# Performance work log

Hardware: AMD Instinct MI355X
Metric: run time of the kernel (lower is better)

Reference implementation:

```python
import jax, jax.numpy as jnp
import numpy as np

BN_EPS = 1e-5


def setup_inputs() -> dict:
    key = jax.random.key(0)
    ks = jax.random.split(key, 8)
    B, C, H, W = 2, 512, 64, 64
    Ck, Cv = 256, 256
    x = jax.random.normal(ks[0], (B, C, H, W), jnp.float32)
    # f_key/f_query shared 1x1 conv (kaiming, relu)
    wk = jax.random.normal(ks[1], (Ck, C), jnp.float32) * (2.0 / C) ** 0.5
    bk = jnp.zeros((Ck,), jnp.float32)
    bn_gamma = jax.random.uniform(ks[2], (Ck,), jnp.float32, 0.5, 1.5)
    bn_beta = jax.random.normal(ks[3], (Ck,), jnp.float32) * 0.1
    bn_mean = jax.random.normal(ks[4], (Ck,), jnp.float32) * 0.1
    bn_var = jax.random.uniform(ks[5], (Ck,), jnp.float32, 0.5, 1.5)
    # f_value: 3x3 conv then 1x1 conv
    wv1 = jax.random.normal(ks[6], (Cv, C, 3, 3), jnp.float32) * (2.0 / (C * 9)) ** 0.5
    bv1 = jnp.zeros((Cv,), jnp.float32)
    wv2 = jax.random.normal(ks[7], (Cv, Cv), jnp.float32) * (2.0 / Cv) ** 0.5
    bv2 = jnp.zeros((Cv,), jnp.float32)
    return dict(x=x, wk=wk, bk=bk, bn_gamma=bn_gamma, bn_beta=bn_beta,
                bn_mean=bn_mean, bn_var=bn_var, wv1=wv1, bv1=bv1, wv2=wv2, bv2=bv2)


def reference(x, wk, bk, bn_gamma, bn_beta, bn_mean, bn_var, wv1, bv1, wv2, bv2):
    B, C, H, W = x.shape
    Ck, Cv = wk.shape[0], wv1.shape[0]
    N = H * W
    # f_key == f_query: 1x1 conv + BN (inference form) + ReLU
    feat = jnp.einsum('oc,bchw->bohw', wk, x) + bk[:, None, None]
    scale_bn = (bn_gamma / jnp.sqrt(bn_var + BN_EPS))
    feat = (feat - bn_mean[:, None, None]) * scale_bn[:, None, None] + bn_beta[:, None, None]
    feat = jax.nn.relu(feat).reshape(B, Ck, N)  # [B, Ck, N]
    # sim_map = softmax(Ck^-0.5 * Q^T K); Q and K are the same tensor
    sim_map = jax.nn.softmax(jnp.einsum('bcn,bcm->bnm', feat, feat) * (Ck ** -0.5), axis=-1)
    # f_value: conv3x3 + relu + conv1x1 + relu
    v = jax.lax.conv_general_dilated(x, wv1, (1, 1), 'SAME',
                                     dimension_numbers=('NCHW', 'OIHW', 'NCHW'))
    v = jax.nn.relu(v + bv1[:, None, None])
    v = jax.nn.relu(jnp.einsum('oc,bchw->bohw', wv2, v) + bv2[:, None, None])
    v = v.reshape(B, Cv, N)  # [B, Cv, N]
    context = jnp.einsum('bnm,bcm->bcn', sim_map, v).reshape(B, Cv, H, W)
    return context, sim_map
```

## Files before the change

kernel.cpp:

```cpp
#include <hip/hip_runtime.h>
#include <hip/hip_bf16.h>
#include <stdint.h>

typedef unsigned short u16_t;
typedef __attribute__((ext_vector_type(8))) short short8;
typedef __attribute__((ext_vector_type(4))) float f32x4;
typedef __attribute__((ext_vector_type(4))) unsigned short us4;

__device__ __forceinline__ float bf2f(u16_t u) {
  union { unsigned int i; float f; } c; c.i = ((unsigned int)u) << 16; return c.f;
}
__device__ __forceinline__ u16_t f2bf(float f) {
  union { float f; unsigned int i; } c; c.f = f;
  unsigned int x = c.i;
  unsigned int r = x + 0x7fffu + ((x >> 16) & 1u);
  return (u16_t)(r >> 16);
}

__device__ __forceinline__ void gload_lds16(const u16_t* g, u16_t* l) {
  __builtin_amdgcn_global_load_lds(
      (const __attribute__((address_space(1))) void*)g,
      (__attribute__((address_space(3))) void*)(unsigned int)(uintptr_t)l,
      16, 0, 0);
}

struct Seg {
  const u16_t* Ah;
  const u16_t* Al;
  const u16_t* Bh;
  const u16_t* Bl;
  int boff;
};

struct GemmArgs {
  Seg segs[9];
  int nseg;
  int segs_per_split;
  int K;
  int ldA, ldB;
  long long sA, sB;
  float alpha;
  float* outf;
  long long sOut;
  long long sSplit;
  int ldT;
};

template<int BM, int BN, int MODE, bool PADB, bool SYMM>
__global__ __launch_bounds__(256, 4) void gemm_tn(GemmArgs args) {
  constexpr int FM = BM / 32, FN = BN / 32;
  __shared__ __align__(16) u16_t lAh[4][BM][8];
  __shared__ __align__(16) u16_t lAl[(MODE == 0) ? 4 : 1][BM][8];
  __shared__ __align__(16) u16_t lBh[4][BN][8];
  __shared__ __align__(16) u16_t lBl[(MODE <= 1) ? 4 : 1][BN][8];
  const int tid = threadIdx.x;
  const int wave = tid >> 6, lane = tid & 63;
  const int lhi = lane >> 4, llo = lane & 15;
  const int wr = wave >> 1, wc = wave & 1;
  int nt, mt, b, split;
  if (SYMM) {
    b = blockIdx.z; split = 0;
    int t = blockIdx.x, r = 0;
    while (t >= 32 - r) { t -= 32 - r; ++r; }
    mt = r; nt = r + t;
  } else {
    nt = blockIdx.x; mt = blockIdx.y;
    b = blockIdx.z & 1; split = blockIdx.z >> 1;
  }
  const int row0 = mt * BM, col0 = nt * BN;

  f32x4 acc[FM][FN];
  const f32x4 zero4 = {0.f, 0.f, 0.f, 0.f};
#pragma unroll
  for (int i = 0; i < FM; ++i)
#pragma unroll
    for (int j = 0; j < FN; ++j) acc[i][j] = zero4;

  constexpr int RA = BM / 64;
  constexpr int RB = BN / 64;
  u16_t* aflat_h = &lAh[0][0][0];
  u16_t* aflat_l = &lAl[0][0][0];
  u16_t* bflat_h = &lBh[0][0][0];
  u16_t* bflat_l = &lBl[0][0][0];

  const int s0 = split * args.segs_per_split;
  int s1 = s0 + args.segs_per_split;
  if (s1 > args.nseg) s1 = args.nseg;

  for (int s = s0; s < s1; ++s) {
    const u16_t* Abh = args.segs[s].Ah + (size_t)b * args.sA;
    const u16_t* Abl = args.segs[s].Al + (size_t)b * args.sA;
    const u16_t* Bbh = args.segs[s].Bh + (size_t)b * args.sB;
    const u16_t* Bbl = args.segs[s].Bl + (size_t)b * args.sB;
    const int boff = args.segs[s].boff;
    for (int k0 = 0; k0 < args.K; k0 += 32) {
      __syncthreads();
#pragma unroll
      for (int r = 0; r < RA; ++r) {
        int idx = (r * 4 + wave) * 64 + lane;
        int chunk = idx / BM, m = idx % BM;
        size_t goff = (size_t)(row0 + m) * args.ldA + (k0 + chunk * 8);
        gload_lds16(Abh + goff, aflat_h + (size_t)((r * 4 + wave) * 64) * 8);
        if (MODE == 0)
          gload_lds16(Abl + goff, aflat_l + (size_t)((r * 4 + wave) * 64) * 8);
      }
#pragma unroll
      for (int r = 0; r < RB; ++r) {
        int idx = (r * 4 + wave) * 64 + lane;
        int chunk = idx / BN, n = idx % BN;
        long long rowi;
        if (PADB) {
          int gn = col0 + n;
          rowi = (long long)((gn >> 6) + 1) * 66 + (gn & 63) + 1 + boff;
        } else {
          rowi = col0 + n;
        }
        size_t goff = (size_t)rowi * args.ldB + (k0 + chunk * 8);
        gload_lds16(Bbh + goff, bflat_h + (size_t)((r * 4 + wave) * 64) * 8);
        if (MODE <= 1)
          gload_lds16(Bbl + goff, bflat_l + (size_t)((r * 4 + wave) * 64) * 8);
      }
      __syncthreads();
      short8 afh[FM], afl[FM], bfh[FN], bfl[FN];
#pragma unroll
      for (int i = 0; i < FM; ++i) {
        afh[i] = *(const short8*)&lAh[lhi][wr * (BM / 2) + i * 16 + llo][0];
        if (MODE == 0)
          afl[i] = *(const short8*)&lAl[lhi][wr * (BM / 2) + i * 16 + llo][0];
      }
#pragma unroll
      for (int j = 0; j < FN; ++j) {
        bfh[j] = *(const short8*)&lBh[lhi][wc * (BN / 2) + j * 16 + llo][0];
        if (MODE <= 1)
          bfl[j] = *(const short8*)&lBl[lhi][wc * (BN / 2) + j * 16 + llo][0];
      }
#pragma unroll
      for (int i = 0; i < FM; ++i)
#pragma unroll
        for (int j = 0; j < FN; ++j) {
          f32x4 t = acc[i][j];
          if (MODE <= 1)
            t = __builtin_amdgcn_mfma_f32_16x16x32_bf16(afh[i], bfl[j], t, 0, 0, 0);
          if (MODE == 0)
            t = __builtin_amdgcn_mfma_f32_16x16x32_bf16(afl[i], bfh[j], t, 0, 0, 0);
          t = __builtin_amdgcn_mfma_f32_16x16x32_bf16(afh[i], bfh[j], t, 0, 0, 0);
          acc[i][j] = t;
        }
    }
  }

  float* outp = args.outf + (size_t)split * args.sSplit + (size_t)b * args.sOut;
#pragma unroll
  for (int i = 0; i < FM; ++i) {
    int mb = row0 + wr * (BM / 2) + i * 16 + lhi * 4;
#pragma unroll
    for (int j = 0; j < FN; ++j) {
      int n = col0 + wc * (BN / 2) + j * 16 + llo;
      f32x4 vv = acc[i][j] * args.alpha;
      *(f32x4*)(outp + (size_t)n * args.ldT + mb) = vv;
    }
  }
  if (SYMM) {
    if (nt != mt) {
#pragma unroll
      for (int i = 0; i < FM; ++i) {
        int mb = row0 + wr * (BM / 2) + i * 16 + lhi * 4;
#pragma unroll
        for (int j = 0; j < FN; ++j) {
          int n = col0 + wc * (BN / 2) + j * 16 + llo;
#pragma unroll
          for (int r2 = 0; r2 < 4; ++r2)
            outp[(size_t)(mb + r2) * args.ldT + n] = acc[i][j][r2] * args.alpha;
        }
      }
    }
  }
}

__global__ __launch_bounds__(256) void zeropad(u16_t* __restrict__ xh, u16_t* __restrict__ xl) {
  int rowi = blockIdx.x % 260;
  int b = blockIdx.x / 260;
  int rp;
  if (rowi < 66) rp = rowi;
  else if (rowi < 132) rp = 4290 + (rowi - 66);
  else { int g = (rowi - 132) >> 1; rp = (g + 1) * 66 + ((rowi - 132) & 1) * 65; }
  size_t base = ((size_t)b * 4356 + rp) * 512;
  int t = threadIdx.x;
  const us4 z = {0, 0, 0, 0};
  if (t < 128) *(us4*)(xh + base + (size_t)t * 4) = z;
  else *(us4*)(xl + base + (size_t)(t - 128) * 4) = z;
}

template<int LDT, bool PER_COL>
__global__ __launch_bounds__(256) void reduce_split(
    const float* __restrict__ part, long long sSplit, int ns,
    const float* __restrict__ scale, const float* __restrict__ bias,
    u16_t* __restrict__ oh, u16_t* __restrict__ ol, long long total) {
  long long i = ((long long)blockIdx.x * 256 + threadIdx.x) * 4;
  if (i >= total) return;
  f32x4 s = *(const f32x4*)(part + i);
  for (int p = 1; p < ns; ++p) s += *(const f32x4*)(part + (size_t)p * sSplit + i);
  f32x4 v;
  if (PER_COL) {
    int c = (int)(i & (LDT - 1));
    f32x4 bi = *(const f32x4*)(bias + c);
    if (scale) { f32x4 sc = *(const f32x4*)(scale + c); v = s * sc + bi; }
    else v = s + bi;
  } else {
    int r = (int)((i / LDT) & 255);
    float bi = bias[r];
    v = s + bi;
  }
  us4 h, l;
#pragma unroll
  for (int c2 = 0; c2 < 4; ++c2) {
    float vv = v[c2] > 0.f ? v[c2] : 0.f;
    u16_t hh = f2bf(vv);
    h[c2] = hh;
    l[c2] = f2bf(vv - bf2f(hh));
  }
  *(us4*)(oh + i) = h;
  if (ol) *(us4*)(ol + i) = l;
}

__global__ __launch_bounds__(256) void reduce_split_f32(
    const float* __restrict__ part, long long sSplit, int ns,
    float* __restrict__ out, long long total) {
  long long i = ((long long)blockIdx.x * 256 + threadIdx.x) * 4;
  if (i >= total) return;
  f32x4 s = *(const f32x4*)(part + i);
  for (int p = 1; p < ns; ++p) s += *(const f32x4*)(part + (size_t)p * sSplit + i);
  *(f32x4*)(out + i) = s;
}

__global__ __launch_bounds__(256) void softmax_k(float* S, u16_t* P) {
  const int row = blockIdx.x;
  float* Sr = S + (size_t)row * 4096;
  u16_t* Pr = P + (size_t)row * 4096;
  const int t = threadIdx.x;
  const int wave = t >> 6;
  f32x4 v[4];
  float vmax = -3.4e38f;
#pragma unroll
  for (int i = 0; i < 4; ++i) {
    v[i] = ((const f32x4*)Sr)[t + i * 256];
#pragma unroll
    for (int c = 0; c < 4; ++c) vmax = fmaxf(vmax, v[i][c]);
  }
#pragma unroll
  for (int off = 32; off; off >>= 1) vmax = fmaxf(vmax, __shfl_xor(vmax, off));
  __shared__ float red[4];
  if ((t & 63) == 0) red[wave] = vmax;
  __syncthreads();
  vmax = fmaxf(fmaxf(red[0], red[1]), fmaxf(red[2], red[3]));
  float sum = 0.f;
#pragma unroll
  for (int i = 0; i < 4; ++i)
#pragma unroll
    for (int c = 0; c < 4; ++c) { v[i][c] = __expf(v[i][c] - vmax); sum += v[i][c]; }
#pragma unroll
  for (int off = 32; off; off >>= 1) sum += __shfl_xor(sum, off);
  __shared__ float red2[4];
  if ((t & 63) == 0) red2[wave] = sum;
  __syncthreads();
  sum = red2[0] + red2[1] + red2[2] + red2[3];
  float rs = 1.0f / sum;
#pragma unroll
  for (int i = 0; i < 4; ++i) {
    f32x4 o = v[i] * rs;
    ((f32x4*)Sr)[t + i * 256] = o;
    us4 pb;
#pragma unroll
    for (int c = 0; c < 4; ++c) pb[c] = f2bf(o[c]);
    ((us4*)Pr)[t + i * 256] = pb;
  }
}

__global__ __launch_bounds__(256) void xprep(const float* __restrict__ x,
                                             u16_t* __restrict__ xh, u16_t* __restrict__ xl) {
  __shared__ float tile[64][65];
  const int b = blockIdx.z, c0 = blockIdx.y * 64, n0 = blockIdx.x * 64;
  const float* xb = x + ((size_t)b * 512 + c0) * 4096 + n0;
  const int t = threadIdx.x;
  const int tr = t >> 6, tc = t & 63;
#pragma unroll
  for (int rr = 0; rr < 16; ++rr) {
    int ci = tr + rr * 4;
    tile[ci][tc] = xb[(size_t)ci * 4096 + tc];
  }
  __syncthreads();
#pragma unroll
  for (int rr = 0; rr < 16; ++rr) {
    int nj = rr * 4 + tr;
    float v = tile[tc][nj];
    size_t rp = (size_t)(blockIdx.x + 1) * 66 + nj + 1;
    size_t o = ((size_t)b * 4356 + rp) * 512 + c0 + tc;
    u16_t hh = f2bf(v);
    xh[o] = hh;
    xl[o] = f2bf(v - bf2f(hh));
  }
}

__global__ __launch_bounds__(256) void wprep(const float* __restrict__ wv1,
                                             u16_t* __restrict__ wh, u16_t* __restrict__ wl) {
  size_t i = (size_t)blockIdx.x * 256 + threadIdx.x;
  const size_t total = 9ull * 256 * 512;
  if (i >= total) return;
  int tp = (int)(i / (256 * 512));
  int rem = (int)(i % (256 * 512));
  int o = rem / 512, c = rem % 512;
  float v = wv1[((size_t)o * 512 + c) * 9 + tp];
  u16_t hh = f2bf(v);
  wh[i] = hh;
  wl[i] = f2bf(v - bf2f(hh));
}

__global__ __launch_bounds__(256) void splitk(const float* __restrict__ s,
                                              u16_t* __restrict__ h, u16_t* __restrict__ l, int n) {
  int i = blockIdx.x * 256 + threadIdx.x;
  if (i < n) {
    float v = s[i];
    u16_t hh = f2bf(v);
    h[i] = hh;
    l[i] = f2bf(v - bf2f(hh));
  }
}

__global__ __launch_bounds__(256) void bnprep(const float* g, const float* be, const float* mu,
                                              const float* var, const float* bk,
                                              float* sA, float* sB) {
  int i = threadIdx.x;
  float s = g[i] * rsqrtf(var[i] + 1e-5f);
  sA[i] = s;
  sB[i] = (bk[i] - mu[i]) * s + be[i];
}

extern "C" void kernel_launch(void* const* d_in, const int* in_sizes, int n_in,
                              void* d_out, int out_size, void* d_ws, size_t ws_size,
                              hipStream_t stream) {
  (void)in_sizes; (void)n_in; (void)out_size; (void)ws_size;
  const float* x   = (const float*)d_in[0];
  const float* wk  = (const float*)d_in[1];
  const float* bk  = (const float*)d_in[2];
  const float* gam = (const float*)d_in[3];
  const float* bet = (const float*)d_in[4];
  const float* mu  = (const float*)d_in[5];
  const float* var = (const float*)d_in[6];
  const float* wv1 = (const float*)d_in[7];
  const float* bv1 = (const float*)d_in[8];
  const float* wv2 = (const float*)d_in[9];
  const float* bv2 = (const float*)d_in[10];

  const int B = 2;
  const size_t XT_E  = (size_t)B * 4356 * 512;
  const size_t WK_E  = 256 * 512;
  const size_t WV1_E = 9ull * 256 * 512;
  const size_t WV2_E = 256 * 256;
  const size_t FT_E  = (size_t)B * 4096 * 256;
  const size_t P_E   = (size_t)B * 4096 * 4096;

  size_t off = 0;
  auto carve = [&](size_t bytes) -> char* {
    off = (off + 255) & ~(size_t)255;
    char* p = (char*)d_ws + off;
    off += bytes;
    return p;
  };
  u16_t* xh  = (u16_t*)carve(XT_E * 2);
  u16_t* xl  = (u16_t*)carve(XT_E * 2);
  u16_t* wkh = (u16_t*)carve(WK_E * 2);
  u16_t* wkl = (u16_t*)carve(WK_E * 2);
  u16_t* w1h = (u16_t*)carve(WV1_E * 2);
  u16_t* w1l = (u16_t*)carve(WV1_E * 2);
  u16_t* w2h = (u16_t*)carve(WV2_E * 2);
  u16_t* w2l = (u16_t*)carve(WV2_E * 2);
  u16_t* fth = (u16_t*)carve(FT_E * 2);
  u16_t* ftl = (u16_t*)carve(FT_E * 2);
  u16_t* v1h = (u16_t*)carve(FT_E * 2);
  u16_t* v1l = (u16_t*)carve(FT_E * 2);
  u16_t* vh  = (u16_t*)carve(FT_E * 2);
  u16_t* vl  = (u16_t*)carve(FT_E * 2);
  u16_t* Pb  = (u16_t*)carve(P_E * 2);
  float* bnA = (float*)carve(256 * 4);
  float* bnB = (float*)carve(256 * 4);

  float* big_part = (float*)Pb;
  float* pv_part  = (float*)d_ws;

  float* ctx = (float*)d_out;
  float* sim = (float*)d_out + (size_t)B * 256 * 4096;

  const long long FT_LL = (long long)FT_E;

  zeropad<<<520, 256, 0, stream>>>(xh, xl);
  bnprep<<<1, 256, 0, stream>>>(gam, bet, mu, var, bk, bnA, bnB);
  splitk<<<(int)((WK_E + 255) / 256), 256, 0, stream>>>(wk, wkh, wkl, (int)WK_E);
  splitk<<<(int)((WV2_E + 255) / 256), 256, 0, stream>>>(wv2, w2h, w2l, (int)WV2_E);
  wprep<<<(int)((WV1_E + 255) / 256), 256, 0, stream>>>(wv1, w1h, w1l);
  xprep<<<dim3(64, 8, 2), 256, 0, stream>>>(x, xh, xl);

  {
    GemmArgs a = {};
    a.segs[0] = {wkh,       wkl,       xh,       xl,       0};
    a.segs[1] = {wkh + 256, wkl + 256, xh + 256, xl + 256, 0};
    a.nseg = 2; a.segs_per_split = 1; a.K = 256; a.ldA = 512; a.ldB = 512;
    a.sA = 0; a.sB = (long long)4356 * 512; a.alpha = 1.f;
    a.outf = big_part; a.sOut = (long long)4096 * 256; a.sSplit = FT_LL; a.ldT = 256;
    gemm_tn<64, 128, 0, true, false><<<dim3(32, 4, 4), 256, 0, stream>>>(a);
    reduce_split<256, true><<<2048, 256, 0, stream>>>(big_part, FT_LL, 2, bnA, bnB, fth, ftl, FT_LL);
  }
  {
    GemmArgs a = {};
    a.segs[0] = {fth, ftl, fth, ftl, 0};
    a.nseg = 1; a.segs_per_split = 1; a.K = 256; a.ldA = 256; a.ldB = 256;
    a.sA = (long long)4096 * 256; a.sB = (long long)4096 * 256; a.alpha = 0.0625f;
    a.outf = sim; a.sOut = (long long)4096 * 4096; a.sSplit = 0; a.ldT = 4096;
    gemm_tn<128, 128, 0, false, true><<<dim3(528, 1, 2), 256, 0, stream>>>(a);
  }
  {
    GemmArgs a = {};
    for (int ty = 0; ty < 3; ++ty)
      for (int tx = 0; tx < 3; ++tx) {
        int tp = ty * 3 + tx;
        int boff = (ty - 1) * 66 + (tx - 1);
        a.segs[tp] = {w1h + (size_t)tp * 131072, nullptr, xh, nullptr, boff};
      }
    a.nseg = 9; a.segs_per_split = 1; a.K = 512; a.ldA = 512; a.ldB = 512;
    a.sA = 0; a.sB = (long long)4356 * 512; a.alpha = 1.f;
    a.outf = big_part; a.sOut = (long long)4096 * 256; a.sSplit = FT_LL; a.ldT = 256;
    gemm_tn<128, 128, 2, true, false><<<dim3(32, 2, 18), 256, 0, stream>>>(a);
    reduce_split<256, true><<<2048, 256, 0, stream>>>(big_part, FT_LL, 9, nullptr, bv1, v1h, v1l, FT_LL);
  }
  {
    GemmArgs a = {};
    a.segs[0] = {v1h,       v1l,       w2h,       w2l,       0};
    a.segs[1] = {v1h + 128, v1l + 128, w2h + 128, w2l + 128, 0};
    a.nseg = 2; a.segs_per_split = 1; a.K = 128; a.ldA = 256; a.ldB = 256;
    a.sA = (long long)4096 * 256; a.sB = 0; a.alpha = 1.f;
    a.outf = big_part; a.sOut = (long long)256 * 4096; a.sSplit = FT_LL; a.ldT = 4096;
    gemm_tn<128, 64, 0, false, false><<<dim3(4, 32, 4), 256, 0, stream>>>(a);
    reduce_split<4096, false><<<2048, 256, 0, stream>>>(big_part, FT_LL, 2, nullptr, bv2, vh, nullptr, FT_LL);
  }
  softmax_k<<<B * 4096, 256, 0, stream>>>(sim, Pb);
  {
    GemmArgs a = {};
    for (int q = 0; q < 4; ++q)
      a.segs[q] = {Pb + (size_t)q * 1024, nullptr, vh + (size_t)q * 1024, nullptr, 0};
    a.nseg = 4; a.segs_per_split = 1; a.K = 1024; a.ldA = 4096; a.ldB = 4096;
    a.sA = (long long)4096 * 4096; a.sB = (long long)256 * 4096; a.alpha = 1.f;
    a.outf = pv_part; a.sOut = (long long)256 * 4096; a.sSplit = FT_LL; a.ldT = 4096;
    gemm_tn<128, 128, 2, false, false><<<dim3(2, 32, 8), 256, 0, stream>>>(a);
    reduce_split_f32<<<2048, 256, 0, stream>>>(pv_part, FT_LL, 4, ctx, FT_LL);
  }
  (void)vl; (void)w1l;
}
```

Baseline: 312.7 us.

## Fuse weight prep kernels, coalesce symmetric transpose store, trim sim precision and splits

Merges bnprep, two splitk and wprep launches into one prep_all kernel and stops writing the unused low part of wv1. The mirrored half of the symmetric sim GEMM is now staged through shared memory so the transposed store is written as coalesced float4 rows instead of strided scalars. The sim GEMM drops from 3-term to 2-term split-bf16 MFMA, and the 3x3 conv GEMM now does two taps per split, giving 5 partial buffers instead of 9. Together these cut launches, MFMA work and reduction traffic, at the cost of slightly lower sim precision and less parallelism in the conv GEMM.

```diff
diff --git a/kernel.cpp b/kernel.cpp
--- a/kernel.cpp
+++ b/kernel.cpp
@@ -49,10 +49,18 @@
 template<int BM, int BN, int MODE, bool PADB, bool SYMM>
 __global__ __launch_bounds__(256, 4) void gemm_tn(GemmArgs args) {
   constexpr int FM = BM / 32, FN = BN / 32;
-  __shared__ __align__(16) u16_t lAh[4][BM][8];
-  __shared__ __align__(16) u16_t lAl[(MODE == 0) ? 4 : 1][BM][8];
-  __shared__ __align__(16) u16_t lBh[4][BN][8];
-  __shared__ __align__(16) u16_t lBl[(MODE <= 1) ? 4 : 1][BN][8];
+  constexpr int AH_E = 4 * BM * 8;
+  constexpr int AL_E = (MODE == 0) ? 4 * BM * 8 : 8;
+  constexpr int BH_E = 4 * BN * 8;
+  constexpr int BL_E = (MODE <= 1) ? 4 * BN * 8 : 8;
+  constexpr int SM_E = AH_E + AL_E + BH_E + BL_E;
+  static_assert(!SYMM || (size_t)SM_E * 2 >= 32 * 132 * 4, "tbuf alias too small");
+  __shared__ __align__(16) u16_t smem[SM_E];
+  u16_t* aflat_h = smem;
+  u16_t* aflat_l = smem + AH_E;
+  u16_t* bflat_h = smem + AH_E + AL_E;
+  u16_t* bflat_l = smem + AH_E + AL_E + BH_E;
+
   const int tid = threadIdx.x;
   const int wave = tid >> 6, lane = tid & 63;
   const int lhi = lane >> 4, llo = lane & 15;
@@ -78,10 +86,6 @@
 
   constexpr int RA = BM / 64;
   constexpr int RB = BN / 64;
-  u16_t* aflat_h = &lAh[0][0][0];
-  u16_t* aflat_l = &lAl[0][0][0];
-  u16_t* bflat_h = &lBh[0][0][0];
-  u16_t* bflat_l = &lBl[0][0][0];
 
   const int s0 = split * args.segs_per_split;
   int s1 = s0 + args.segs_per_split;
@@ -124,15 +128,15 @@
       short8 afh[FM], afl[FM], bfh[FN], bfl[FN];
 #pragma unroll
       for (int i = 0; i < FM; ++i) {
-        afh[i] = *(const short8*)&lAh[lhi][wr * (BM / 2) + i * 16 + llo][0];
+        afh[i] = *(const short8*)(aflat_h + ((size_t)lhi * BM + wr * (BM / 2) + i * 16 + llo) * 8);
         if (MODE == 0)
-          afl[i] = *(const short8*)&lAl[lhi][wr * (BM / 2) + i * 16 + llo][0];
+          afl[i] = *(const short8*)(aflat_l + ((size_t)lhi * BM + wr * (BM / 2) + i * 16 + llo) * 8);
       }
 #pragma unroll
       for (int j = 0; j < FN; ++j) {
-        bfh[j] = *(const short8*)&lBh[lhi][wc * (BN / 2) + j * 16 + llo][0];
+        bfh[j] = *(const short8*)(bflat_h + ((size_t)lhi * BN + wc * (BN / 2) + j * 16 + llo) * 8);
         if (MODE <= 1)
-          bfl[j] = *(const short8*)&lBl[lhi][wc * (BN / 2) + j * 16 + llo][0];
+          bfl[j] = *(const short8*)(bflat_l + ((size_t)lhi * BN + wc * (BN / 2) + j * 16 + llo) * 8);
       }
 #pragma unroll
       for (int i = 0; i < FM; ++i)
@@ -162,15 +166,27 @@
   }
   if (SYMM) {
     if (nt != mt) {
+      float* tb = (float*)smem;
 #pragma unroll
       for (int i = 0; i < FM; ++i) {
-        int mb = row0 + wr * (BM / 2) + i * 16 + lhi * 4;
+        __syncthreads();
 #pragma unroll
         for (int j = 0; j < FN; ++j) {
-          int n = col0 + wc * (BN / 2) + j * 16 + llo;
-#pragma unroll
-          for (int r2 = 0; r2 < 4; ++r2)
-            outp[(size_t)(mb + r2) * args.ldT + n] = acc[i][j][r2] * args.alpha;
+#pragma unroll
+          for (int r2 = 0; r2 < 4; ++r2) {
+            int trow = wr * 16 + lhi * 4 + r2;
+            int tcol = wc * 64 + j * 16 + llo;
+            tb[trow * 132 + tcol] = acc[i][j][r2] * args.alpha;
+          }
+        }
+        __syncthreads();
+#pragma unroll
+        for (int it = 0; it < 4; ++it) {
+          int idx = it * 256 + tid;
+          int row = idx >> 5, c4 = idx & 31;
+          int mg = row0 + (row >> 4) * 64 + i * 16 + (row & 15);
+          f32x4 v4 = *(f32x4*)&tb[row * 132 + c4 * 4];
+          *(f32x4*)(outp + (size_t)mg * args.ldT + col0 + c4 * 4) = v4;
         }
       }
     }
@@ -301,38 +317,41 @@
   }
 }
 
-__global__ __launch_bounds__(256) void wprep(const float* __restrict__ wv1,
-                                             u16_t* __restrict__ wh, u16_t* __restrict__ wl) {
-  size_t i = (size_t)blockIdx.x * 256 + threadIdx.x;
-  const size_t total = 9ull * 256 * 512;
-  if (i >= total) return;
-  int tp = (int)(i / (256 * 512));
-  int rem = (int)(i % (256 * 512));
-  int o = rem / 512, c = rem % 512;
-  float v = wv1[((size_t)o * 512 + c) * 9 + tp];
-  u16_t hh = f2bf(v);
-  wh[i] = hh;
-  wl[i] = f2bf(v - bf2f(hh));
-}
-
-__global__ __launch_bounds__(256) void splitk(const float* __restrict__ s,
-                                              u16_t* __restrict__ h, u16_t* __restrict__ l, int n) {
-  int i = blockIdx.x * 256 + threadIdx.x;
-  if (i < n) {
-    float v = s[i];
+__global__ __launch_bounds__(256) void prep_all(
+    const float* __restrict__ wk, const float* __restrict__ wv2, const float* __restrict__ wv1,
+    const float* __restrict__ g, const float* __restrict__ be, const float* __restrict__ mu,
+    const float* __restrict__ var, const float* __restrict__ bkb,
+    u16_t* __restrict__ wkh, u16_t* __restrict__ wkl,
+    u16_t* __restrict__ w2h, u16_t* __restrict__ w2l,
+    u16_t* __restrict__ w1h, float* __restrict__ bnA, float* __restrict__ bnB) {
+  long long i = (long long)blockIdx.x * 256 + threadIdx.x;
+  if (i < 256) {
+    float s = g[i] * rsqrtf(var[i] + 1e-5f);
+    bnA[i] = s;
+    bnB[i] = (bkb[i] - mu[i]) * s + be[i];
+    return;
+  }
+  i -= 256;
+  if (i < 131072) {
+    float v = wk[i];
     u16_t hh = f2bf(v);
-    h[i] = hh;
-    l[i] = f2bf(v - bf2f(hh));
-  }
-}
-
-__global__ __launch_bounds__(256) void bnprep(const float* g, const float* be, const float* mu,
-                                              const float* var, const float* bk,
-                                              float* sA, float* sB) {
-  int i = threadIdx.x;
-  float s = g[i] * rsqrtf(var[i] + 1e-5f);
-  sA[i] = s;
-  sB[i] = (bk[i] - mu[i]) * s + be[i];
+    wkh[i] = hh; wkl[i] = f2bf(v - bf2f(hh));
+    return;
+  }
+  i -= 131072;
+  if (i < 65536) {
+    float v = wv2[i];
+    u16_t hh = f2bf(v);
+    w2h[i] = hh; w2l[i] = f2bf(v - bf2f(hh));
+    return;
+  }
+  i -= 65536;
+  if (i < 1179648) {
+    int tp = (int)(i / (256 * 512));
+    int rem = (int)(i % (256 * 512));
+    int o = rem / 512, c = rem % 512;
+    w1h[i] = f2bf(wv1[((size_t)o * 512 + c) * 9 + tp]);
+  }
 }
 
 extern "C" void kernel_launch(void* const* d_in, const int* in_sizes, int n_in,
@@ -393,10 +412,8 @@
   const long long FT_LL = (long long)FT_E;
 
   zeropad<<<520, 256, 0, stream>>>(xh, xl);
-  bnprep<<<1, 256, 0, stream>>>(gam, bet, mu, var, bk, bnA, bnB);
-  splitk<<<(int)((WK_E + 255) / 256), 256, 0, stream>>>(wk, wkh, wkl, (int)WK_E);
-  splitk<<<(int)((WV2_E + 255) / 256), 256, 0, stream>>>(wv2, w2h, w2l, (int)WV2_E);
-  wprep<<<(int)((WV1_E + 255) / 256), 256, 0, stream>>>(wv1, w1h, w1l);
+  prep_all<<<5377, 256, 0, stream>>>(wk, wv2, wv1, gam, bet, mu, var, bk,
+                                     wkh, wkl, w2h, w2l, w1h, bnA, bnB);
   xprep<<<dim3(64, 8, 2), 256, 0, stream>>>(x, xh, xl);
 
   {
@@ -411,11 +428,11 @@
   }
   {
     GemmArgs a = {};
-    a.segs[0] = {fth, ftl, fth, ftl, 0};
+    a.segs[0] = {fth, nullptr, fth, ftl, 0};
     a.nseg = 1; a.segs_per_split = 1; a.K = 256; a.ldA = 256; a.ldB = 256;
     a.sA = (long long)4096 * 256; a.sB = (long long)4096 * 256; a.alpha = 0.0625f;
     a.outf = sim; a.sOut = (long long)4096 * 4096; a.sSplit = 0; a.ldT = 4096;
-    gemm_tn<128, 128, 0, false, true><<<dim3(528, 1, 2), 256, 0, stream>>>(a);
+    gemm_tn<128, 128, 1, false, true><<<dim3(528, 1, 2), 256, 0, stream>>>(a);
   }
   {
     GemmArgs a = {};
@@ -425,11 +442,11 @@
         int boff = (ty - 1) * 66 + (tx - 1);
         a.segs[tp] = {w1h + (size_t)tp * 131072, nullptr, xh, nullptr, boff};
       }
-    a.nseg = 9; a.segs_per_split = 1; a.K = 512; a.ldA = 512; a.ldB = 512;
+    a.nseg = 9; a.segs_per_split = 2; a.K = 512; a.ldA = 512; a.ldB = 512;
     a.sA = 0; a.sB = (long long)4356 * 512; a.alpha = 1.f;
     a.outf = big_part; a.sOut = (long long)4096 * 256; a.sSplit = FT_LL; a.ldT = 256;
-    gemm_tn<128, 128, 2, true, false><<<dim3(32, 2, 18), 256, 0, stream>>>(a);
-    reduce_split<256, true><<<2048, 256, 0, stream>>>(big_part, FT_LL, 9, nullptr, bv1, v1h, v1l, FT_LL);
+    gemm_tn<128, 128, 2, true, false><<<dim3(32, 2, 10), 256, 0, stream>>>(a);
+    reduce_split<256, true><<<2048, 256, 0, stream>>>(big_part, FT_LL, 5, nullptr, bv1, v1h, v1l, FT_LL);
   }
   {
     GemmArgs a = {};
```

New measurement: 281.1 us. 10.1% less time.
